# Performance work log

Hardware: AMD Instinct MI355X
Metric: run time of the kernel (lower is better)

Reference implementation:

```python
import jax, jax.numpy as jnp
import numpy as np

D_MODEL = 1024
N_HEADS = 16
HEAD_DIM = D_MODEL // N_HEADS
NEG_INF = -1e9


def setup_inputs() -> dict:
    key = jax.random.key(0)
    ks = jax.random.split(key, 6)
    B, T, C = 4, 2048, D_MODEL
    x = jax.random.normal(ks[0], (B, T, C), dtype=jnp.float32)
    # causal mask, broadcastable over batch and heads
    mask = jnp.tril(jnp.ones((T, T), dtype=jnp.int32))[None, None]
    scale = 1.0 / np.sqrt(C)
    W_qkv = jax.random.normal(ks[1], (3 * C, C), dtype=jnp.float32) * scale
    b_qkv = jnp.zeros((3 * C,), dtype=jnp.float32)
    W_out = jax.random.normal(ks[2], (C, C), dtype=jnp.float32) * scale
    b_out = jnp.zeros((C,), dtype=jnp.float32)
    return {"x": x, "mask": mask, "W_qkv": W_qkv, "b_qkv": b_qkv,
            "W_out": W_out, "b_out": b_out}


def reference(x, mask, W_qkv, b_qkv, W_out, b_out):
    B, T, C = x.shape
    H, D = N_HEADS, HEAD_DIM
    qkv = x @ W_qkv.T + b_qkv                      # [B, T, 3C]
    q, k, v = jnp.split(qkv, 3, axis=-1)
    # [B, T, C] -> [B, H, T, D]
    q = q.reshape(B, T, H, D).transpose(0, 2, 1, 3)
    k = k.reshape(B, T, H, D).transpose(0, 2, 1, 3)
    v = v.reshape(B, T, H, D).transpose(0, 2, 1, 3)
    scores = jnp.einsum("bhqd,bhkd->bhqk", q, k) / np.sqrt(D)
    scores = jnp.where(mask == 0, NEG_INF, scores)
    att = jax.nn.softmax(scores, axis=-1)          # dropout p=0 (eval)
    out = jnp.einsum("bhqk,bhkd->bhqd", att, v)    # [B, H, T, D]
    out = out.transpose(0, 2, 1, 3).reshape(B, T, C)
    return out @ W_out.T + b_out
```

## Files before the change

### kernel.cpp

```cpp
#include <hip/hip_runtime.h>
#include <hip/hip_bf16.h>

typedef unsigned short u16;
typedef unsigned int u32;
using short8 = __attribute__((ext_vector_type(8))) short;
using f32x4  = __attribute__((ext_vector_type(4))) float;
using f32x16 = __attribute__((ext_vector_type(16))) float;
using uint2v = __attribute__((ext_vector_type(2))) u32;

#define T_SEQ 2048
#define C_DIM 1024
#define NH 16
#define HD 64

#if __has_builtin(__builtin_amdgcn_exp2f)
#define EXP2(x) __builtin_amdgcn_exp2f(x)
#else
#define EXP2(x) exp2f(x)
#endif

__device__ __forceinline__ u16 f2bf(float f) {
    unsigned int u = __float_as_uint(f);
    unsigned int r = (u + 0x7fffu + ((u >> 16) & 1u)) >> 16;
    return (u16)r;
}
__device__ __forceinline__ u32 cvtpk(float lo, float hi) {
    u32 r;
    asm("v_cvt_pk_bf16_f32 %0, %1, %2" : "=v"(r) : "v"(lo), "v"(hi));
    return r;
}
__device__ __forceinline__ short8 mk8(u32 a, u32 b, u32 c, u32 d) {
    union { u32 u[4]; short8 s; } t;
    t.u[0] = a; t.u[1] = b; t.u[2] = c; t.u[3] = d;
    return t.s;
}
__device__ __forceinline__ void gl_lds16(const u16* g, u16* l) {
    __builtin_amdgcn_global_load_lds(
        (const __attribute__((address_space(1))) unsigned int*)g,
        (__attribute__((address_space(3))) unsigned int*)l, 16, 0, 0);
}
template <int N> __device__ __forceinline__ void s_vmcnt();
template <> __device__ __forceinline__ void s_vmcnt<0>() {
    asm volatile("s_waitcnt vmcnt(0)" ::: "memory");
}
template <> __device__ __forceinline__ void s_vmcnt<4>() {
    asm volatile("s_waitcnt vmcnt(4)" ::: "memory");
}
__device__ __forceinline__ void BAR() {
    asm volatile("" ::: "memory");
    __builtin_amdgcn_s_barrier();
    asm volatile("" ::: "memory");
}

__global__ __launch_bounds__(256) void cvt_f32_bf16(const float* __restrict__ in,
                                                    u16* __restrict__ out, int n8) {
    int i = blockIdx.x * blockDim.x + threadIdx.x;
    if (i >= n8) return;
    const float4* p = (const float4*)in + (size_t)i * 2;
    float4 a = p[0], b = p[1];
    short8 o;
    o[0] = (short)f2bf(a.x); o[1] = (short)f2bf(a.y);
    o[2] = (short)f2bf(a.z); o[3] = (short)f2bf(a.w);
    o[4] = (short)f2bf(b.x); o[5] = (short)f2bf(b.y);
    o[6] = (short)f2bf(b.z); o[7] = (short)f2bf(b.w);
    *(short8*)(out + (size_t)i * 8) = o;
}

template <int EPI, int NX>
__global__ __launch_bounds__(256) void gemm_bt(const u16* __restrict__ A,
                                               const u16* __restrict__ Bt,
                                               const float* __restrict__ bias,
                                               u16* __restrict__ qb, u16* __restrict__ kb,
                                               u16* __restrict__ vtb, float* __restrict__ Cf,
                                               int M, int N, int K) {
    __shared__ __align__(16) u16 Al[2][128][32];
    __shared__ __align__(16) u16 Bl[2][128][32];
    const int tid = threadIdx.x;
    const int lane = tid & 63, wid = tid >> 6;
    const int li = lane & 15, g = lane >> 4;
    const int wr = (wid >> 1) * 64, wc = (wid & 1) * 64;

    const int bid = blockIdx.x;
    const int xcd = bid & 7;
    const int r_ = bid >> 3;
    const int xq = r_ >> 5;
    const int rem = r_ & 31;
    const int yloc = rem >> 2, xr = rem & 3;
    const size_t m0 = (size_t)(xcd * 8 + yloc) * 128;
    const size_t n0 = (size_t)(xq * 4 + xr) * 128;

    const int srow = lane >> 2;
    const int sch = (lane & 3) ^ ((srow >> 1) & 3);
    const u16* aA = A + (m0 + wid * 32 + srow) * (size_t)K + sch * 8;
    const u16* aB = Bt + (n0 + wid * 32 + srow) * (size_t)K + sch * 8;

    f32x4 acc[4][4] = {};
    const int nt = K / 32;

    auto STAGE = [&](int buf, int k0) {
        gl_lds16(aA + k0, &Al[buf][wid * 32][0]);
        gl_lds16(aA + 16 * (size_t)K + k0, &Al[buf][wid * 32 + 16][0]);
        gl_lds16(aB + k0, &Bl[buf][wid * 32][0]);
        gl_lds16(aB + 16 * (size_t)K + k0, &Bl[buf][wid * 32 + 16][0]);
    };

    STAGE(0, 0);
#pragma unroll 2
    for (int t = 0; t < nt; ++t) {
        if (t + 1 < nt) { STAGE((t + 1) & 1, (t + 1) * 32); s_vmcnt<4>(); }
        else            { s_vmcnt<0>(); }
        BAR();
        short8 af[4], bf[4];
#pragma unroll
        for (int i = 0; i < 4; i++) {
            int row = wr + i * 16 + li;
            af[i] = *(const short8*)&Al[t & 1][row][(g ^ ((row >> 1) & 3)) * 8];
        }
#pragma unroll
        for (int i = 0; i < 4; i++) {
            int row = wc + i * 16 + li;
            bf[i] = *(const short8*)&Bl[t & 1][row][(g ^ ((row >> 1) & 3)) * 8];
        }
        __builtin_amdgcn_s_setprio(1);
#pragma unroll
        for (int mi = 0; mi < 4; mi++)
#pragma unroll
            for (int ni = 0; ni < 4; ni++)
                acc[mi][ni] = __builtin_amdgcn_mfma_f32_16x16x32_bf16(af[mi], bf[ni],
                                                                      acc[mi][ni], 0, 0, 0);
        __builtin_amdgcn_s_setprio(0);
        BAR();
    }

#pragma unroll
    for (int mi = 0; mi < 4; mi++)
#pragma unroll
        for (int ni = 0; ni < 4; ni++) {
            size_t col = n0 + wc + ni * 16 + li;
            size_t row0 = m0 + wr + mi * 16 + g * 4;
            if (EPI == 0) {
                int which = (int)(col >> 10);
                int rem2 = (int)(col & 1023);
                int h = rem2 >> 6, d = rem2 & 63;
                size_t b = row0 >> 11, t0v = row0 & 2047;
                float bv = bias[col];
                if (which == 2) {
                    ushort4 o4;
                    o4.x = f2bf(acc[mi][ni][0] + bv);
                    o4.y = f2bf(acc[mi][ni][1] + bv);
                    o4.z = f2bf(acc[mi][ni][2] + bv);
                    o4.w = f2bf(acc[mi][ni][3] + bv);
                    *(ushort4*)(vtb + (((b * NH) + h) * (size_t)HD + d) * T_SEQ + t0v) = o4;
                } else {
                    u16* dst = (which == 0) ? qb : kb;
                    float sc = (which == 0) ? 0.18033688f : 1.0f;
#pragma unroll
                    for (int r = 0; r < 4; r++)
                        dst[(((b * NH) + h) * T_SEQ + t0v + r) * HD + d] =
                            f2bf((acc[mi][ni][r] + bv) * sc);
                }
            } else {
                float bv = bias[col];
#pragma unroll
                for (int r = 0; r < 4; r++)
                    Cf[(row0 + r) * (size_t)N + col] = acc[mi][ni][r] + bv;
            }
        }
}

__global__ __launch_bounds__(256) void attn_fwd2(const u16* __restrict__ Q,
                                                 const u16* __restrict__ K,
                                                 const u16* __restrict__ Vt,
                                                 u16* __restrict__ O) {
    __shared__ __align__(16) u16 KL[2][64 * 64];
    __shared__ __align__(16) u16 VL[2][64 * 64];
    const int tid = threadIdx.x;
    const int lane = tid & 63, wid = tid >> 6;
    const int l31 = lane & 31, hi = lane >> 5;

    const int wg = blockIdx.x;
    const int j = wg >> 8, c = wg & 255;
    const int xcd = c & 7, m = c >> 3;
    const int bh = (xcd << 3) | (m >> 2);
    const int v = m & 3;
    const int qt = (j == 0) ? (15 - v) : (j == 1) ? v : (j == 2) ? (11 - v) : (v + 4);

    const size_t bhT = (size_t)bh * T_SEQ;
    const int srow8 = lane >> 3, sch = lane & 7;
    const int b = bh >> 4, h = bh & 15;
    const int x7 = l31 & 7;

    const int q0 = qt * 128;
    const int qw0 = q0 + wid * 32;
    const int nkt = 2 * qt + 2;

    short8 qf[4];
    {
        const u16* qp = Q + (bhT + qw0 + l31) * HD + hi * 8;
#pragma unroll
        for (int s = 0; s < 4; s++) qf[s] = *(const short8*)(qp + s * 16);
    }

    f32x16 o0 = {}, o1 = {};
    float l_run = 0.f;

#pragma unroll
    for (int i = 0; i < 2; i++) {
        int row = wid * 16 + i * 8 + srow8;
        int ch = sch ^ (row & 7);
        gl_lds16(K + (bhT + row) * HD + ch * 8, &KL[0][(wid * 16 + i * 8) * 64]);
        gl_lds16(Vt + ((size_t)bh * HD + row) * T_SEQ + ch * 8,
                 &VL[0][(wid * 16 + i * 8) * 64]);
    }

    for (int kt = 0; kt < nkt; kt++) {
        __syncthreads();
        if (kt + 1 < nkt) {
            const int kv0n = (kt + 1) * 64;
            const int nb = (kt + 1) & 1;
#pragma unroll
            for (int i = 0; i < 2; i++) {
                int row = wid * 16 + i * 8 + srow8;
                int ch = sch ^ (row & 7);
                gl_lds16(K + (bhT + kv0n + row) * HD + ch * 8,
                         &KL[nb][(wid * 16 + i * 8) * 64]);
                gl_lds16(Vt + ((size_t)bh * HD + row) * T_SEQ + kv0n + ch * 8,
                         &VL[nb][(wid * 16 + i * 8) * 64]);
            }
        }
        const int kv0 = kt * 64;
        if (kv0 > qw0) continue;
        const u16* KLb = KL[kt & 1];
        const u16* VLb = VL[kt & 1];

        f32x16 s0 = {}, s1 = {};
        __builtin_amdgcn_s_setprio(1);
#pragma unroll
        for (int sl = 0; sl < 4; sl++) {
            int ch = ((sl * 2 + hi) ^ x7) * 8;
            short8 ka = *(const short8*)&KLb[l31 * 64 + ch];
            s0 = __builtin_amdgcn_mfma_f32_32x32x16_bf16(ka, qf[sl], s0, 0, 0, 0);
            short8 kb2 = *(const short8*)&KLb[(32 + l31) * 64 + ch];
            s1 = __builtin_amdgcn_mfma_f32_32x32x16_bf16(kb2, qf[sl], s1, 0, 0, 0);
        }
        __builtin_amdgcn_s_setprio(0);

        const int qg = qw0 + l31;
        if (kv0 + 63 > qw0) {
#pragma unroll
            for (int r = 0; r < 16; r++) {
                int kvr = kv0 + (r & 3) + 8 * (r >> 2) + 4 * hi;
                if (kvr > qg) s0[r] = -1e30f;
                if (kvr + 32 > qg) s1[r] = -1e30f;
            }
        }

        float ls = 0.f;
#pragma unroll
        for (int r = 0; r < 16; r++) {
            float p0 = EXP2(s0[r]);
            float p1 = EXP2(s1[r]);
            s0[r] = p0; s1[r] = p1;
            ls += p0 + p1;
        }
        ls += __shfl_xor(ls, 32);
        l_run += ls;

        {
            u32 c0 = cvtpk(s0[0], s0[1]),   c1 = cvtpk(s0[2], s0[3]),
                c2 = cvtpk(s0[4], s0[5]),   c3 = cvtpk(s0[6], s0[7]),
                c4 = cvtpk(s0[8], s0[9]),   c5 = cvtpk(s0[10], s0[11]),
                c6 = cvtpk(s0[12], s0[13]), c7 = cvtpk(s0[14], s0[15]);
            uint2v wA = __builtin_amdgcn_permlane32_swap(c0, c2, false, false);
            uint2v wB = __builtin_amdgcn_permlane32_swap(c1, c3, false, false);
            uint2v wC = __builtin_amdgcn_permlane32_swap(c4, c6, false, false);
            uint2v wD = __builtin_amdgcn_permlane32_swap(c5, c7, false, false);
            short8 paA = mk8(wA[0], wB[0], wA[1], wB[1]);
            short8 paB = mk8(wC[0], wD[0], wC[1], wD[1]);
            __builtin_amdgcn_s_setprio(1);
#pragma unroll
            for (int sl = 0; sl < 2; sl++) {
                short8 pa = (sl == 0) ? paA : paB;
                int ch = ((sl * 2 + hi) ^ x7) * 8;
                short8 va = *(const short8*)&VLb[l31 * 64 + ch];
                o0 = __builtin_amdgcn_mfma_f32_32x32x16_bf16(pa, va, o0, 0, 0, 0);
                short8 vb2 = *(const short8*)&VLb[(32 + l31) * 64 + ch];
                o1 = __builtin_amdgcn_mfma_f32_32x32x16_bf16(pa, vb2, o1, 0, 0, 0);
            }
            __builtin_amdgcn_s_setprio(0);
        }
        {
            u32 c0 = cvtpk(s1[0], s1[1]),   c1 = cvtpk(s1[2], s1[3]),
                c2 = cvtpk(s1[4], s1[5]),   c3 = cvtpk(s1[6], s1[7]),
                c4 = cvtpk(s1[8], s1[9]),   c5 = cvtpk(s1[10], s1[11]),
                c6 = cvtpk(s1[12], s1[13]), c7 = cvtpk(s1[14], s1[15]);
            uint2v wA = __builtin_amdgcn_permlane32_swap(c0, c2, false, false);
            uint2v wB = __builtin_amdgcn_permlane32_swap(c1, c3, false, false);
            uint2v wC = __builtin_amdgcn_permlane32_swap(c4, c6, false, false);
            uint2v wD = __builtin_amdgcn_permlane32_swap(c5, c7, false, false);
            short8 paC = mk8(wA[0], wB[0], wA[1], wB[1]);
            short8 paD = mk8(wC[0], wD[0], wC[1], wD[1]);
            __builtin_amdgcn_s_setprio(1);
#pragma unroll
            for (int sl = 2; sl < 4; sl++) {
                short8 pa = (sl == 2) ? paC : paD;
                int ch = ((sl * 2 + hi) ^ x7) * 8;
                short8 va = *(const short8*)&VLb[l31 * 64 + ch];
                o0 = __builtin_amdgcn_mfma_f32_32x32x16_bf16(pa, va, o0, 0, 0, 0);
                short8 vb2 = *(const short8*)&VLb[(32 + l31) * 64 + ch];
                o1 = __builtin_amdgcn_mfma_f32_32x32x16_bf16(pa, vb2, o1, 0, 0, 0);
            }
            __builtin_amdgcn_s_setprio(0);
        }
    }

    const float inv = 1.0f / l_run;
#pragma unroll
    for (int r = 0; r < 16; r++) {
        int qr = (r & 3) + 8 * (r >> 2) + 4 * hi;
        float invr = __shfl(inv, qr);
        int t = q0 + wid * 32 + qr;
        size_t rowoff = ((size_t)b * T_SEQ + t) * C_DIM + h * HD;
        O[rowoff + l31]      = f2bf(o0[r] * invr);
        O[rowoff + 32 + l31] = f2bf(o1[r] * invr);
    }
}

extern "C" void kernel_launch(void* const* d_in, const int* in_sizes, int n_in,
                              void* d_out, int out_size, void* d_ws, size_t ws_size,
                              hipStream_t stream) {
    const float* x     = (const float*)d_in[0];
    const float* W_qkv = (const float*)d_in[2];
    const float* b_qkv = (const float*)d_in[3];
    const float* W_out = (const float*)d_in[4];
    const float* b_out = (const float*)d_in[5];
    float* out = (float*)d_out;

    char* w = (char*)d_ws;
    u16* xb    = (u16*)(w);
    u16* wqkvb = (u16*)(w + 16777216);
    u16* woutb = (u16*)(w + 23068672);
    u16* qb    = (u16*)(w + 25165824);
    u16* kb    = (u16*)(w + 41943040);
    u16* vtb   = (u16*)(w + 58720256);
    u16* attnb = xb;

    cvt_f32_bf16<<<4096, 256, 0, stream>>>(x, xb, 1048576);
    cvt_f32_bf16<<<1536, 256, 0, stream>>>(W_qkv, wqkvb, 393216);
    cvt_f32_bf16<<<512, 256, 0, stream>>>(W_out, woutb, 131072);

    gemm_bt<0, 24><<<1536, 256, 0, stream>>>(xb, wqkvb, b_qkv, qb, kb, vtb, nullptr,
                                             8192, 3072, 1024);

    attn_fwd2<<<1024, 256, 0, stream>>>(qb, kb, vtb, attnb);

    gemm_bt<1, 8><<<512, 256, 0, stream>>>(attnb, woutb, b_out, nullptr, nullptr,
                                           nullptr, out, 8192, 1024, 1024);
}
```

Before: 160.5 us.

## Use explicit vmcnt waits and barriers in attention loop; merge weight conversions

The attention inner loop drops the single __syncthreads at the loop top. Instead it issues the next K/V async loads, waits with s_vmcnt only until the current tile's loads have landed, and places raw barriers before compute and after compute to guard buffer reuse. This lets the prefetch for the next tile stay in flight during compute rather than being drained by a full sync, at the cost of a second barrier per iteration. The two weight-conversion launches are also merged into one kernel to save a launch.

```diff
diff --git a/kernel.cpp b/kernel.cpp
--- a/kernel.cpp
+++ b/kernel.cpp
@@ -64,6 +64,26 @@
     o[4] = (short)f2bf(b.x); o[5] = (short)f2bf(b.y);
     o[6] = (short)f2bf(b.z); o[7] = (short)f2bf(b.w);
     *(short8*)(out + (size_t)i * 8) = o;
+}
+
+__global__ __launch_bounds__(256) void cvt_w2(const float* __restrict__ a,
+                                              u16* __restrict__ oa, int na8,
+                                              const float* __restrict__ b,
+                                              u16* __restrict__ ob, int nb8) {
+    int i = blockIdx.x * blockDim.x + threadIdx.x;
+    const float* src;
+    u16* dst;
+    if (i < na8) { src = a; dst = oa; }
+    else if (i < na8 + nb8) { src = b; dst = ob; i -= na8; }
+    else return;
+    const float4* p = (const float4*)src + (size_t)i * 2;
+    float4 x = p[0], y = p[1];
+    short8 o;
+    o[0] = (short)f2bf(x.x); o[1] = (short)f2bf(x.y);
+    o[2] = (short)f2bf(x.z); o[3] = (short)f2bf(x.w);
+    o[4] = (short)f2bf(y.x); o[5] = (short)f2bf(y.y);
+    o[6] = (short)f2bf(y.z); o[7] = (short)f2bf(y.w);
+    *(short8*)(dst + (size_t)i * 8) = o;
 }
 
 template <int EPI, int NX>
@@ -214,7 +234,6 @@
     }
 
     for (int kt = 0; kt < nkt; kt++) {
-        __syncthreads();
         if (kt + 1 < nkt) {
             const int kv0n = (kt + 1) * 64;
             const int nb = (kt + 1) & 1;
@@ -227,91 +246,98 @@
                 gl_lds16(Vt + ((size_t)bh * HD + row) * T_SEQ + kv0n + ch * 8,
                          &VL[nb][(wid * 16 + i * 8) * 64]);
             }
-        }
+            s_vmcnt<4>();
+        } else {
+            s_vmcnt<0>();
+        }
+        BAR();
+
         const int kv0 = kt * 64;
-        if (kv0 > qw0) continue;
-        const u16* KLb = KL[kt & 1];
-        const u16* VLb = VL[kt & 1];
-
-        f32x16 s0 = {}, s1 = {};
-        __builtin_amdgcn_s_setprio(1);
-#pragma unroll
-        for (int sl = 0; sl < 4; sl++) {
-            int ch = ((sl * 2 + hi) ^ x7) * 8;
-            short8 ka = *(const short8*)&KLb[l31 * 64 + ch];
-            s0 = __builtin_amdgcn_mfma_f32_32x32x16_bf16(ka, qf[sl], s0, 0, 0, 0);
-            short8 kb2 = *(const short8*)&KLb[(32 + l31) * 64 + ch];
-            s1 = __builtin_amdgcn_mfma_f32_32x32x16_bf16(kb2, qf[sl], s1, 0, 0, 0);
-        }
-        __builtin_amdgcn_s_setprio(0);
-
-        const int qg = qw0 + l31;
-        if (kv0 + 63 > qw0) {
+        if (kv0 <= qw0) {
+            const u16* KLb = KL[kt & 1];
+            const u16* VLb = VL[kt & 1];
+
+            f32x16 s0 = {}, s1 = {};
+            __builtin_amdgcn_s_setprio(1);
+#pragma unroll
+            for (int sl = 0; sl < 4; sl++) {
+                int ch = ((sl * 2 + hi) ^ x7) * 8;
+                short8 ka = *(const short8*)&KLb[l31 * 64 + ch];
+                s0 = __builtin_amdgcn_mfma_f32_32x32x16_bf16(ka, qf[sl], s0, 0, 0, 0);
+                short8 kb2 = *(const short8*)&KLb[(32 + l31) * 64 + ch];
+                s1 = __builtin_amdgcn_mfma_f32_32x32x16_bf16(kb2, qf[sl], s1, 0, 0, 0);
+            }
+            __builtin_amdgcn_s_setprio(0);
+
+            const int qg = qw0 + l31;
+            if (kv0 + 63 > qw0) {
+#pragma unroll
+                for (int r = 0; r < 16; r++) {
+                    int kvr = kv0 + (r & 3) + 8 * (r >> 2) + 4 * hi;
+                    if (kvr > qg) s0[r] = -1e30f;
+                    if (kvr + 32 > qg) s1[r] = -1e30f;
+                }
+            }
+
+            float ls = 0.f;
 #pragma unroll
             for (int r = 0; r < 16; r++) {
-                int kvr = kv0 + (r & 3) + 8 * (r >> 2) + 4 * hi;
-                if (kvr > qg) s0[r] = -1e30f;
-                if (kvr + 32 > qg) s1[r] = -1e30f;
-            }
-        }
-
-        float ls = 0.f;
-#pragma unroll
-        for (int r = 0; r < 16; r++) {
-            float p0 = EXP2(s0[r]);
-            float p1 = EXP2(s1[r]);
-            s0[r] = p0; s1[r] = p1;
-            ls += p0 + p1;
-        }
-        ls += __shfl_xor(ls, 32);
-        l_run += ls;
-
-        {
-            u32 c0 = cvtpk(s0[0], s0[1]),   c1 = cvtpk(s0[2], s0[3]),
-                c2 = cvtpk(s0[4], s0[5]),   c3 = cvtpk(s0[6], s0[7]),
-                c4 = cvtpk(s0[8], s0[9]),   c5 = cvtpk(s0[10], s0[11]),
-                c6 = cvtpk(s0[12], s0[13]), c7 = cvtpk(s0[14], s0[15]);
-            uint2v wA = __builtin_amdgcn_permlane32_swap(c0, c2, false, false);
-            uint2v wB = __builtin_amdgcn_permlane32_swap(c1, c3, false, false);
-            uint2v wC = __builtin_amdgcn_permlane32_swap(c4, c6, false, false);
-            uint2v wD = __builtin_amdgcn_permlane32_swap(c5, c7, false, false);
-            short8 paA = mk8(wA[0], wB[0], wA[1], wB[1]);
-            short8 paB = mk8(wC[0], wD[0], wC[1], wD[1]);
-            __builtin_amdgcn_s_setprio(1);
-#pragma unroll
-            for (int sl = 0; sl < 2; sl++) {
-                short8 pa = (sl == 0) ? paA : paB;
-                int ch = ((sl * 2 + hi) ^ x7) * 8;
-                short8 va = *(const short8*)&VLb[l31 * 64 + ch];
-                o0 = __builtin_amdgcn_mfma_f32_32x32x16_bf16(pa, va, o0, 0, 0, 0);
-                short8 vb2 = *(const short8*)&VLb[(32 + l31) * 64 + ch];
-                o1 = __builtin_amdgcn_mfma_f32_32x32x16_bf16(pa, vb2, o1, 0, 0, 0);
-            }
-            __builtin_amdgcn_s_setprio(0);
-        }
-        {
-            u32 c0 = cvtpk(s1[0], s1[1]),   c1 = cvtpk(s1[2], s1[3]),
-                c2 = cvtpk(s1[4], s1[5]),   c3 = cvtpk(s1[6], s1[7]),
-                c4 = cvtpk(s1[8], s1[9]),   c5 = cvtpk(s1[10], s1[11]),
-                c6 = cvtpk(s1[12], s1[13]), c7 = cvtpk(s1[14], s1[15]);
-            uint2v wA = __builtin_amdgcn_permlane32_swap(c0, c2, false, false);
-            uint2v wB = __builtin_amdgcn_permlane32_swap(c1, c3, false, false);
-            uint2v wC = __builtin_amdgcn_permlane32_swap(c4, c6, false, false);
-            uint2v wD = __builtin_amdgcn_permlane32_swap(c5, c7, false, false);
-            short8 paC = mk8(wA[0], wB[0], wA[1], wB[1]);
-            short8 paD = mk8(wC[0], wD[0], wC[1], wD[1]);
-            __builtin_amdgcn_s_setprio(1);
-#pragma unroll
-            for (int sl = 2; sl < 4; sl++) {
-                short8 pa = (sl == 2) ? paC : paD;
-                int ch = ((sl * 2 + hi) ^ x7) * 8;
-                short8 va = *(const short8*)&VLb[l31 * 64 + ch];
-                o0 = __builtin_amdgcn_mfma_f32_32x32x16_bf16(pa, va, o0, 0, 0, 0);
-                short8 vb2 = *(const short8*)&VLb[(32 + l31) * 64 + ch];
-                o1 = __builtin_amdgcn_mfma_f32_32x32x16_bf16(pa, vb2, o1, 0, 0, 0);
-            }
-            __builtin_amdgcn_s_setprio(0);
-        }
+                float p0 = EXP2(s0[r]);
+                float p1 = EXP2(s1[r]);
+                s0[r] = p0; s1[r] = p1;
+                ls += p0 + p1;
+            }
+            ls += __shfl_xor(ls, 32);
+            l_run += ls;
+
+            {
+                u32 c0 = cvtpk(s0[0], s0[1]),   c1 = cvtpk(s0[2], s0[3]),
+                    c2 = cvtpk(s0[4], s0[5]),   c3 = cvtpk(s0[6], s0[7]),
+                    c4 = cvtpk(s0[8], s0[9]),   c5 = cvtpk(s0[10], s0[11]),
+                    c6 = cvtpk(s0[12], s0[13]), c7 = cvtpk(s0[14], s0[15]);
+                uint2v wA = __builtin_amdgcn_permlane32_swap(c0, c2, false, false);
+                uint2v wB = __builtin_amdgcn_permlane32_swap(c1, c3, false, false);
+                uint2v wC = __builtin_amdgcn_permlane32_swap(c4, c6, false, false);
+                uint2v wD = __builtin_amdgcn_permlane32_swap(c5, c7, false, false);
+                short8 paA = mk8(wA[0], wB[0], wA[1], wB[1]);
+                short8 paB = mk8(wC[0], wD[0], wC[1], wD[1]);
+                __builtin_amdgcn_s_setprio(1);
+#pragma unroll
+                for (int sl = 0; sl < 2; sl++) {
+                    short8 pa = (sl == 0) ? paA : paB;
+                    int ch = ((sl * 2 + hi) ^ x7) * 8;
+                    short8 va = *(const short8*)&VLb[l31 * 64 + ch];
+                    o0 = __builtin_amdgcn_mfma_f32_32x32x16_bf16(pa, va, o0, 0, 0, 0);
+                    short8 vb2 = *(const short8*)&VLb[(32 + l31) * 64 + ch];
+                    o1 = __builtin_amdgcn_mfma_f32_32x32x16_bf16(pa, vb2, o1, 0, 0, 0);
+                }
+                __builtin_amdgcn_s_setprio(0);
+            }
+            {
+                u32 c0 = cvtpk(s1[0], s1[1]),   c1 = cvtpk(s1[2], s1[3]),
+                    c2 = cvtpk(s1[4], s1[5]),   c3 = cvtpk(s1[6], s1[7]),
+                    c4 = cvtpk(s1[8], s1[9]),   c5 = cvtpk(s1[10], s1[11]),
+                    c6 = cvtpk(s1[12], s1[13]), c7 = cvtpk(s1[14], s1[15]);
+                uint2v wA = __builtin_amdgcn_permlane32_swap(c0, c2, false, false);
+                uint2v wB = __builtin_amdgcn_permlane32_swap(c1, c3, false, false);
+                uint2v wC = __builtin_amdgcn_permlane32_swap(c4, c6, false, false);
+                uint2v wD = __builtin_amdgcn_permlane32_swap(c5, c7, false, false);
+                short8 paC = mk8(wA[0], wB[0], wA[1], wB[1]);
+                short8 paD = mk8(wC[0], wD[0], wC[1], wD[1]);
+                __builtin_amdgcn_s_setprio(1);
+#pragma unroll
+                for (int sl = 2; sl < 4; sl++) {
+                    short8 pa = (sl == 2) ? paC : paD;
+                    int ch = ((sl * 2 + hi) ^ x7) * 8;
+                    short8 va = *(const short8*)&VLb[l31 * 64 + ch];
+                    o0 = __builtin_amdgcn_mfma_f32_32x32x16_bf16(pa, va, o0, 0, 0, 0);
+                    short8 vb2 = *(const short8*)&VLb[(32 + l31) * 64 + ch];
+                    o1 = __builtin_amdgcn_mfma_f32_32x32x16_bf16(pa, vb2, o1, 0, 0, 0);
+                }
+                __builtin_amdgcn_s_setprio(0);
+            }
+        }
+        BAR();
     }
 
     const float inv = 1.0f / l_run;
@@ -346,8 +372,7 @@
     u16* attnb = xb;
 
     cvt_f32_bf16<<<4096, 256, 0, stream>>>(x, xb, 1048576);
-    cvt_f32_bf16<<<1536, 256, 0, stream>>>(W_qkv, wqkvb, 393216);
-    cvt_f32_bf16<<<512, 256, 0, stream>>>(W_out, woutb, 131072);
+    cvt_w2<<<2048, 256, 0, stream>>>(W_qkv, wqkvb, 393216, W_out, woutb, 131072);
 
     gemm_bt<0, 24><<<1536, 256, 0, stream>>>(xb, wqkvb, b_qkv, qb, kb, vtb, nullptr,
                                              8192, 3072, 1024);
```

After: 160.0 us. No clear change (-0.3%).
